# Optimization experiments

Measured on AMD Instinct MI355X. Metric: run time of the kernel, lower is better.

## Reference

```python
import jax, jax.numpy as jnp
import numpy as np

IN_FEATS = 64
OUT_FEATS = 64
HID = IN_FEATS * OUT_FEATS  # 4096, LSTM hidden size
N_NODES = 50000
N_EDGES = 800000
T = 3
NEG_SLOPE = 0.2


def setup_inputs() -> dict:
    key = jax.random.key(0)
    ks = jax.random.split(key, 12)
    node_embs = jax.random.normal(ks[0], (T, N_NODES, IN_FEATS), dtype=jnp.float32)
    mask = jax.random.normal(ks[1], (T, N_NODES), dtype=jnp.float32)
    edge_index = jax.random.randint(ks[2], (T, 2, N_EDGES), 0, N_NODES, dtype=jnp.int64)
    edge_weight = jax.random.uniform(ks[3], (T, N_EDGES), dtype=jnp.float32)
    # LSTMCell params (torch layout): gates order i,f,g,o
    s_ih = 1.0 / np.sqrt(HID)
    W_ih = jax.random.uniform(ks[4], (4 * HID, IN_FEATS), minval=-s_ih, maxval=s_ih, dtype=jnp.float32)
    W_hh = jax.random.uniform(ks[5], (4 * HID, HID), minval=-s_ih, maxval=s_ih, dtype=jnp.float32)
    b_ih = jax.random.uniform(ks[6], (4 * HID,), minval=-s_ih, maxval=s_ih, dtype=jnp.float32)
    b_hh = jax.random.uniform(ks[7], (4 * HID,), minval=-s_ih, maxval=s_ih, dtype=jnp.float32)
    # GCN init weights, uniform(-1/sqrt(out), 1/sqrt(out))
    s_w = 1.0 / np.sqrt(OUT_FEATS)
    W0 = jax.random.uniform(ks[8], (IN_FEATS, OUT_FEATS), minval=-s_w, maxval=s_w, dtype=jnp.float32)
    # GAT attention vector, split into src/dst halves
    att = jax.random.uniform(ks[9], (2, OUT_FEATS), minval=-s_w, maxval=s_w, dtype=jnp.float32)
    return {"node_embs": node_embs, "mask": mask, "edge_index": edge_index,
            "edge_weight": edge_weight, "W_ih": W_ih, "W_hh": W_hh,
            "b_ih": b_ih, "b_hh": b_hh, "W0": W0, "att": att}


def _lstm_cell(x, h, c, W_ih, W_hh, b_ih, b_hh):
    gates = W_ih @ x + b_ih + W_hh @ h + b_hh  # [4H]
    i, f, g, o = jnp.split(gates, 4)
    c2 = jax.nn.sigmoid(f) * c + jax.nn.sigmoid(i) * jnp.tanh(g)
    h2 = jax.nn.sigmoid(o) * jnp.tanh(c2)
    return h2, c2


def _gat_mp(x, src, dst, edge_w, W, att_l, att_r):
    h = x @ W  # [N, out]
    e = jax.nn.leaky_relu(h[src] @ att_l + h[dst] @ att_r, NEG_SLOPE)  # [E]
    m = jax.ops.segment_max(e, dst, num_segments=N_NODES)
    ex = jnp.exp(e - m[dst])
    denom = jax.ops.segment_sum(ex, dst, num_segments=N_NODES)
    alpha = ex / (denom[dst] + 1e-16)
    msg = (alpha * edge_w)[:, None] * h[src]  # [E, out]
    return jax.ops.segment_sum(msg, dst, num_segments=N_NODES)  # [N, out]


def reference(node_embs, mask, edge_index, edge_weight, W_ih, W_hh, b_ih, b_hh, W0, att):
    att_l, att_r = att[0], att[1]

    def step(carry, xs):
        h, c = carry
        x_t, mask_t, ei_t, ew_t = xs
        # input to weight-evolving LSTM: softmax-weighted node-feature mean -> [in_feats]
        w = jax.nn.softmax(mask_t)
        inp = jnp.einsum('n,nf->f', w, x_t)
        h2, c2 = _lstm_cell(inp, h, c, W_ih, W_hh, b_ih, b_hh)
        W = h2.reshape(IN_FEATS, OUT_FEATS)
        out = _gat_mp(x_t, ei_t[0], ei_t[1], ew_t, W, att_l, att_r)
        return (h2, c2), out

    init = (W0.reshape(-1), jnp.zeros((HID,), dtype=W0.dtype))
    _, out_seq = jax.lax.scan(step, init, (node_embs, mask, edge_index, edge_weight))
    return out_seq  # [T, N, out_feats]
```

## Files before the change

kernel.cpp:

```cpp
#include <hip/hip_runtime.h>
#include <hip/hip_fp16.h>
#include <math.h>

#define NN 50000
#define NE 800000
#define FEAT 64
#define HID 4096
#define NEG_SLOPE 0.2f
#define T_STEPS 3
#define SLOTS 64
#define NB 391
#define CAP 2560
#define CHUNK 4096
#define CHUNKS_PER_STEP ((NE + CHUNK - 1) / CHUNK)
#define FEAT_BLKS ((NN + 255) / 256)

__device__ __forceinline__ int pack_half2(float a, float b) {
    __half2 h = __floats2half2_rn(a, b);
    return *(int*)&h;
}
__device__ __forceinline__ float2 unpack_half2(int v) {
    __half2 h = *(__half2*)&v;
    return __half22float2(h);
}

__global__ void k_init(const float* __restrict__ W0, float* __restrict__ h0, float* __restrict__ c,
                       float* __restrict__ inp_acc, float* __restrict__ sumexp,
                       int* __restrict__ coarse_cnt) {
    int i = blockIdx.x * blockDim.x + threadIdx.x;
    if (i < HID) { h0[i] = W0[i]; c[i] = 0.f; }
    if (i < T_STEPS * FEAT) inp_acc[i] = 0.f;
    if (i < T_STEPS) sumexp[i] = 0.f;
    if (i < T_STEPS * NB) coarse_cnt[i] = 0;
}

__global__ void k_wsum_all(const float* __restrict__ node_embs, const float* __restrict__ mask,
                           float* __restrict__ sumexp, float* __restrict__ inp_acc) {
    int t = blockIdx.x >> 8;
    int blk = blockIdx.x & 255;
    const float* x_t = node_embs + (size_t)t * NN * FEAT;
    const float* mask_t = mask + (size_t)t * NN;
    int lane = threadIdx.x & 63;
    int wib = threadIdx.x >> 6;
    int gw = blk * 4 + wib;
    float acc = 0.f, se = 0.f;
    for (int n = gw; n < NN; n += 1024) {
        float w = expf(mask_t[n]);
        acc += w * x_t[(size_t)n * FEAT + lane];
        se += w;
    }
    __shared__ float sacc[4][FEAT];
    sacc[wib][lane] = acc;
    __syncthreads();
    if (wib == 0)
        atomicAdd(&inp_acc[t * FEAT + lane],
                  sacc[0][lane] + sacc[1][lane] + sacc[2][lane] + sacc[3][lane]);
    if (lane == 0) atomicAdd(&sumexp[t], se);
}

template <bool CVT>
__global__ __launch_bounds__(256) void k_lstm(
    const float* __restrict__ Wih, const float* __restrict__ Whh, __half* __restrict__ Whh_h,
    const float* __restrict__ bih, const float* __restrict__ bhh,
    const float* __restrict__ inp_acc_t, const float* __restrict__ sumexp_t,
    const float* __restrict__ h_old, float* __restrict__ h_new,
    float* __restrict__ c, float* __restrict__ Wbuf_t) {
    int lane = threadIdx.x & 63;
    int u = (blockIdx.x * blockDim.x + threadIdx.x) >> 6;
    if (u >= HID) return;
    float inp_l = inp_acc_t[lane] / (*sumexp_t);
    const float4* h4 = (const float4*)h_old;
    float g4[4];
    #pragma unroll
    for (int gi = 0; gi < 4; ++gi) {
        int row = u + gi * HID;
        float acc = 0.f;
        if (CVT) {
            const float4* wr = (const float4*)(Whh + (size_t)row * HID);
            int2* wh = (int2*)(Whh_h + (size_t)row * HID);
            #pragma unroll
            for (int cc = 0; cc < 16; ++cc) {
                float4 w = wr[cc * 64 + lane];
                float4 hv = h4[cc * 64 + lane];
                acc += w.x * hv.x + w.y * hv.y + w.z * hv.z + w.w * hv.w;
                int2 p;
                p.x = pack_half2(w.x, w.y);
                p.y = pack_half2(w.z, w.w);
                wh[cc * 64 + lane] = p;
            }
        } else {
            const int4* wr = (const int4*)(Whh_h + (size_t)row * HID);
            #pragma unroll
            for (int cc = 0; cc < 8; ++cc) {
                int4 w = wr[cc * 64 + lane];
                float2 wa = unpack_half2(w.x), wb = unpack_half2(w.y);
                float2 wc = unpack_half2(w.z), wd = unpack_half2(w.w);
                float4 hv0 = h4[(cc * 64 + lane) * 2];
                float4 hv1 = h4[(cc * 64 + lane) * 2 + 1];
                acc += wa.x * hv0.x + wa.y * hv0.y + wb.x * hv0.z + wb.y * hv0.w;
                acc += wc.x * hv1.x + wc.y * hv1.y + wd.x * hv1.z + wd.y * hv1.w;
            }
        }
        acc += Wih[(size_t)row * FEAT + lane] * inp_l;
        #pragma unroll
        for (int off = 32; off > 0; off >>= 1) acc += __shfl_xor(acc, off, 64);
        if (lane == 0) g4[gi] = acc + bih[row] + bhh[row];
    }
    if (lane == 0) {
        float si = 1.f / (1.f + expf(-g4[0]));
        float sf = 1.f / (1.f + expf(-g4[1]));
        float so = 1.f / (1.f + expf(-g4[3]));
        float c2 = sf * c[u] + si * tanhf(g4[2]);
        float h2 = so * tanhf(c2);
        c[u] = c2; h_new[u] = h2; Wbuf_t[u] = h2;
    }
}

__global__ __launch_bounds__(256) void k_feat_all(
    const float* __restrict__ node_embs, const float* __restrict__ Wbuf,
    const float* __restrict__ att, __half* __restrict__ hfeat,
    float* __restrict__ al, float* __restrict__ ar) {
    int t = blockIdx.x / FEAT_BLKS;
    int blk = blockIdx.x % FEAT_BLKS;
    __shared__ float Wl[HID];
    __shared__ float attS[2 * FEAT];
    for (int i = threadIdx.x; i < HID; i += 256) Wl[i] = Wbuf[t * HID + i];
    if (threadIdx.x < 2 * FEAT) attS[threadIdx.x] = att[threadIdx.x];
    __syncthreads();
    int n = blk * 256 + threadIdx.x;
    if (n >= NN) return;
    const float* x_t = node_embs + (size_t)t * NN * FEAT;
    float acc[FEAT];
    #pragma unroll
    for (int o = 0; o < FEAT; ++o) acc[o] = 0.f;
    const float4* x4 = (const float4*)(x_t + (size_t)n * FEAT);
    for (int k4 = 0; k4 < 16; ++k4) {
        float4 xv = x4[k4];
        const float* w0 = &Wl[(k4 * 4 + 0) * FEAT];
        const float* w1 = &Wl[(k4 * 4 + 1) * FEAT];
        const float* w2 = &Wl[(k4 * 4 + 2) * FEAT];
        const float* w3 = &Wl[(k4 * 4 + 3) * FEAT];
        #pragma unroll
        for (int o = 0; o < FEAT; ++o)
            acc[o] += xv.x * w0[o] + xv.y * w1[o] + xv.z * w2[o] + xv.w * w3[o];
    }
    float aL = 0.f, aR = 0.f;
    #pragma unroll
    for (int o = 0; o < FEAT; ++o) { aL += acc[o] * attS[o]; aR += acc[o] * attS[FEAT + o]; }
    size_t gn = (size_t)t * NN + n;
    int4* hf = (int4*)(hfeat + gn * FEAT);
    #pragma unroll
    for (int i = 0; i < 8; ++i) {
        int4 v;
        v.x = pack_half2(acc[8 * i + 0], acc[8 * i + 1]);
        v.y = pack_half2(acc[8 * i + 2], acc[8 * i + 3]);
        v.z = pack_half2(acc[8 * i + 4], acc[8 * i + 5]);
        v.w = pack_half2(acc[8 * i + 6], acc[8 * i + 7]);
        hf[i] = v;
    }
    al[gn] = aL; ar[gn] = aR;
}

__global__ __launch_bounds__(256) void k_part(
    const int* __restrict__ edge_index, const float* __restrict__ edge_weight,
    int* __restrict__ coarse_cnt, int2* __restrict__ coarse) {
    int t = blockIdx.x / CHUNKS_PER_STEP;
    int ch = blockIdx.x % CHUNKS_PER_STEP;
    int e0 = ch * CHUNK;
    int eN = (e0 + CHUNK <= NE) ? CHUNK : (NE - e0);
    const int* src = edge_index + (size_t)t * 2 * NE;
    const int* dst = src + NE;
    const float* ew = edge_weight + (size_t)t * NE;
    int tid = threadIdx.x;

    __shared__ int hist[NB], offs[NB], baseg[NB], cursor[NB];
    __shared__ int sc[256];
    __shared__ int2 stag[CHUNK];

    for (int i = tid; i < NB; i += 256) hist[i] = 0;
    __syncthreads();
    for (int k = tid; k < eN; k += 256) {
        int d = dst[e0 + k];
        atomicAdd(&hist[d >> 7], 1);
    }
    __syncthreads();
    int a0 = (2 * tid < NB) ? hist[2 * tid] : 0;
    int a1 = (2 * tid + 1 < NB) ? hist[2 * tid + 1] : 0;
    sc[tid] = a0 + a1;
    __syncthreads();
    for (int off = 1; off < 256; off <<= 1) {
        int v = (tid >= off) ? sc[tid - off] : 0;
        __syncthreads();
        sc[tid] += v;
        __syncthreads();
    }
    int excl = (tid == 0) ? 0 : sc[tid - 1];
    if (2 * tid < NB)     { offs[2 * tid] = excl;      cursor[2 * tid] = excl; }
    if (2 * tid + 1 < NB) { offs[2 * tid + 1] = excl + a0; cursor[2 * tid + 1] = excl + a0; }
    __syncthreads();
    for (int k = tid; k < eN; k += 256) {
        int d = dst[e0 + k], s = src[e0 + k];
        float wv = ew[e0 + k];
        int cb = d >> 7, doff = d & 127;
        int p = atomicAdd(&cursor[cb], 1);
        stag[p] = make_int2(s | (doff << 16) | (cb << 23), __float_as_int(wv));
    }
    __syncthreads();
    for (int cb = tid; cb < NB; cb += 256) {
        int cnum = hist[cb];
        baseg[cb] = cnum ? atomicAdd(&coarse_cnt[t * NB + cb], cnum) : 0;
    }
    __syncthreads();
    for (int j = tid; j < eN; j += 256) {
        int2 r = stag[j];
        int cb = ((unsigned)r.x) >> 23;
        int gpos = baseg[cb] + (j - offs[cb]);
        if (gpos < CAP)
            coarse[((size_t)(t * NB + cb)) * CAP + gpos] = r;
    }
}

__global__ __launch_bounds__(512) void k_gat(
    const int* __restrict__ coarse_cnt, const int2* __restrict__ coarse,
    const float* __restrict__ al, const float* __restrict__ ar,
    const __half* __restrict__ hfeat, float* __restrict__ out) {
    int t = blockIdx.x / NB;
    int cb = blockIdx.x % NB;
    int n0 = cb << 7;
    int tid = threadIdx.x;
    __shared__ int fine[128 * SLOTS];
    __shared__ int fcnt[128];
    for (int i = tid; i < 128; i += 512) fcnt[i] = 0;
    __syncthreads();
    int m = coarse_cnt[t * NB + cb];
    if (m > CAP) m = CAP;
    const int2* reg = coarse + ((size_t)(t * NB + cb)) * CAP;
    for (int k = tid; k < m; k += 512) {
        int2 r = reg[k];
        int doff = (r.x >> 16) & 127;
        int p = atomicAdd(&fcnt[doff], 1);
        if (p < SLOTS) {
            unsigned int eh = (unsigned int)__half_as_ushort(__float2half_rn(__int_as_float(r.y)));
            fine[doff * SLOTS + p] = (r.x & 0xffff) | (int)(eh << 16);
        }
    }
    __syncthreads();
    int lane = tid & 63, w = tid >> 6;
    const float* al_t = al + (size_t)t * NN;
    const __half* hf_t = hfeat + (size_t)t * NN * FEAT;
    int sub = lane >> 4;
    int fl = (lane & 15) * 4;
    for (int doff = w; doff < 128; doff += 8) {
        int row = n0 + doff;
        if (row >= NN) break;
        int cn = fcnt[doff]; if (cn > SLOTS) cn = SLOTS;
        float ard = ar[(size_t)t * NN + row];
        float4 acc = make_float4(0.f, 0.f, 0.f, 0.f);
        float psum = 0.f;
        for (int i = sub; i < cn; i += 4) {
            int r = fine[doff * SLOTS + i];
            int s = r & 0xffff;
            float ewv = __half2float(__ushort_as_half((unsigned short)((unsigned int)r >> 16)));
            float e = al_t[s] + ard;
            e = e >= 0.f ? e : NEG_SLOPE * e;
            float p = expf(e);
            psum += p;
            float pe = p * ewv;
            int2 hv2 = *(const int2*)(hf_t + (size_t)s * FEAT + fl);
            float2 ha = unpack_half2(hv2.x), hb = unpack_half2(hv2.y);
            acc.x += pe * ha.x; acc.y += pe * ha.y;
            acc.z += pe * hb.x; acc.w += pe * hb.y;
        }
        acc.x += __shfl_xor(acc.x, 16, 64); acc.y += __shfl_xor(acc.y, 16, 64);
        acc.z += __shfl_xor(acc.z, 16, 64); acc.w += __shfl_xor(acc.w, 16, 64);
        psum  += __shfl_xor(psum, 16, 64);
        acc.x += __shfl_xor(acc.x, 32, 64); acc.y += __shfl_xor(acc.y, 32, 64);
        acc.z += __shfl_xor(acc.z, 32, 64); acc.w += __shfl_xor(acc.w, 32, 64);
        psum  += __shfl_xor(psum, 32, 64);
        float inv = 1.f / (psum + 1e-16f);
        if (sub == 0)
            *(float4*)(out + ((size_t)t * NN + row) * FEAT + fl) =
                make_float4(acc.x * inv, acc.y * inv, acc.z * inv, acc.w * inv);
    }
}

extern "C" void kernel_launch(void* const* d_in, const int* in_sizes, int n_in,
                              void* d_out, int out_size, void* d_ws, size_t ws_size,
                              hipStream_t stream) {
    const float* node_embs   = (const float*)d_in[0];
    const float* mask        = (const float*)d_in[1];
    const int*   edge_index  = (const int*)d_in[2];
    const float* edge_weight = (const float*)d_in[3];
    const float* Wih         = (const float*)d_in[4];
    const float* Whh         = (const float*)d_in[5];
    const float* bih         = (const float*)d_in[6];
    const float* bhh         = (const float*)d_in[7];
    const float* W0          = (const float*)d_in[8];
    const float* att         = (const float*)d_in[9];
    float* out = (float*)d_out;
    float* ws  = (float*)d_ws;

    float*  h0       = ws;
    float*  h1       = ws + 4096;
    float*  c_state  = ws + 8192;
    float*  sumexp   = ws + 12288;
    float*  inp_acc  = ws + 12292;
    float*  Wbuf     = ws + 12544;
    float*  al       = ws + 24832;
    float*  ar       = ws + 174832;
    int*    ccnt     = (int*)(ws + 324832);
    int2*   coarse   = (int2*)(ws + 326016);
    __half* Whh_h    = (__half*)(ws + 6331776);
    __half* hfeat    = (__half*)(ws + 39886208);

    k_init<<<16, 256, 0, stream>>>(W0, h0, c_state, inp_acc, sumexp, ccnt);
    k_wsum_all<<<T_STEPS * 256, 256, 0, stream>>>(node_embs, mask, sumexp, inp_acc);

    float* hc = h0;
    for (int t = 0; t < T_STEPS; ++t) {
        float* hn = (hc == h0) ? h1 : h0;
        if (t == 0)
            k_lstm<true><<<HID / 4, 256, 0, stream>>>(Wih, Whh, Whh_h, bih, bhh,
                                                      inp_acc + t * FEAT, sumexp + t,
                                                      hc, hn, c_state, Wbuf + (size_t)t * HID);
        else
            k_lstm<false><<<HID / 4, 256, 0, stream>>>(Wih, Whh, Whh_h, bih, bhh,
                                                       inp_acc + t * FEAT, sumexp + t,
                                                       hc, hn, c_state, Wbuf + (size_t)t * HID);
        hc = hn;
    }

    k_feat_all<<<T_STEPS * FEAT_BLKS, 256, 0, stream>>>(node_embs, Wbuf, att, hfeat, al, ar);
    k_part<<<T_STEPS * CHUNKS_PER_STEP, 256, 0, stream>>>(edge_index, edge_weight, ccnt, coarse);
    k_gat<<<T_STEPS * NB, 512, 0, stream>>>(ccnt, coarse, al, ar, hfeat, out);
}
```

Baseline: 354.2 us.

## Merge prep kernels and overlap per-step feature transform with next LSTM step

Edge partitioning, the weighted node mean and a standalone fp32-to-fp16 conversion of W_hh now run as disjoint block ranges of a single prep kernel, so these independent phases share one launch and fill the GPU together. The feature transform for step t is fused into the same launch as the LSTM for step t+1, letting the memory-bound LSTM matvec overlap with the node feature GEMM. Initialization moves to a device memcpy and memset, and the first LSTM step no longer converts W_hh itself. This adds a separate full pass over W_hh for the conversion and makes block scheduling of the mixed launches harder to predict.

```diff
diff --git a/kernel.cpp b/kernel.cpp
--- a/kernel.cpp
+++ b/kernel.cpp
@@ -14,6 +14,9 @@
 #define CHUNK 4096
 #define CHUNKS_PER_STEP ((NE + CHUNK - 1) / CHUNK)
 #define FEAT_BLKS ((NN + 255) / 256)
+#define PART_BLKS (T_STEPS * CHUNKS_PER_STEP)
+#define WSUM_BLKS (T_STEPS * 256)
+#define CVT_BLKS 4096
 
 __device__ __forceinline__ int pack_half2(float a, float b) {
     __half2 h = __floats2half2_rn(a, b);
@@ -24,71 +27,163 @@
     return __half22float2(h);
 }
 
-__global__ void k_init(const float* __restrict__ W0, float* __restrict__ h0, float* __restrict__ c,
-                       float* __restrict__ inp_acc, float* __restrict__ sumexp,
-                       int* __restrict__ coarse_cnt) {
-    int i = blockIdx.x * blockDim.x + threadIdx.x;
-    if (i < HID) { h0[i] = W0[i]; c[i] = 0.f; }
-    if (i < T_STEPS * FEAT) inp_acc[i] = 0.f;
-    if (i < T_STEPS) sumexp[i] = 0.f;
-    if (i < T_STEPS * NB) coarse_cnt[i] = 0;
-}
-
-__global__ void k_wsum_all(const float* __restrict__ node_embs, const float* __restrict__ mask,
-                           float* __restrict__ sumexp, float* __restrict__ inp_acc) {
-    int t = blockIdx.x >> 8;
-    int blk = blockIdx.x & 255;
-    const float* x_t = node_embs + (size_t)t * NN * FEAT;
-    const float* mask_t = mask + (size_t)t * NN;
-    int lane = threadIdx.x & 63;
-    int wib = threadIdx.x >> 6;
-    int gw = blk * 4 + wib;
-    float acc = 0.f, se = 0.f;
-    for (int n = gw; n < NN; n += 1024) {
-        float w = expf(mask_t[n]);
-        acc += w * x_t[(size_t)n * FEAT + lane];
-        se += w;
+__global__ __launch_bounds__(256) void k_prep(
+    const int* __restrict__ edge_index, const float* __restrict__ edge_weight,
+    const float* __restrict__ node_embs, const float* __restrict__ mask,
+    const float* __restrict__ Whh, __half* __restrict__ Whh_h,
+    float* __restrict__ sumexp, float* __restrict__ inp_acc,
+    int* __restrict__ coarse_cnt, int2* __restrict__ coarse) {
+    __shared__ char smem[40448];
+    int bid = blockIdx.x;
+    int tid = threadIdx.x;
+    if (bid < PART_BLKS) {
+        int t = bid / CHUNKS_PER_STEP;
+        int ch = bid % CHUNKS_PER_STEP;
+        int e0 = ch * CHUNK;
+        int eN = (e0 + CHUNK <= NE) ? CHUNK : (NE - e0);
+        const int* src = edge_index + (size_t)t * 2 * NE;
+        const int* dst = src + NE;
+        const float* ew = edge_weight + (size_t)t * NE;
+        int2* stag  = (int2*)smem;
+        int* hist   = (int*)(smem + 32768);
+        int* offs   = (int*)(smem + 34332);
+        int* baseg  = (int*)(smem + 35896);
+        int* cursor = (int*)(smem + 37460);
+        int* sc     = (int*)(smem + 39024);
+        for (int i = tid; i < NB; i += 256) hist[i] = 0;
+        __syncthreads();
+        for (int k = tid; k < eN; k += 256) atomicAdd(&hist[dst[e0 + k] >> 7], 1);
+        __syncthreads();
+        int a0 = (2 * tid < NB) ? hist[2 * tid] : 0;
+        int a1 = (2 * tid + 1 < NB) ? hist[2 * tid + 1] : 0;
+        sc[tid] = a0 + a1;
+        __syncthreads();
+        for (int off = 1; off < 256; off <<= 1) {
+            int v = (tid >= off) ? sc[tid - off] : 0;
+            __syncthreads();
+            sc[tid] += v;
+            __syncthreads();
+        }
+        int excl = (tid == 0) ? 0 : sc[tid - 1];
+        if (2 * tid < NB)     { offs[2 * tid] = excl;          cursor[2 * tid] = excl; }
+        if (2 * tid + 1 < NB) { offs[2 * tid + 1] = excl + a0; cursor[2 * tid + 1] = excl + a0; }
+        __syncthreads();
+        for (int k = tid; k < eN; k += 256) {
+            int d = dst[e0 + k], s = src[e0 + k];
+            float wv = ew[e0 + k];
+            int cb = d >> 7, doff = d & 127;
+            int p = atomicAdd(&cursor[cb], 1);
+            stag[p] = make_int2(s | (doff << 16) | (cb << 23), __float_as_int(wv));
+        }
+        __syncthreads();
+        for (int cb = tid; cb < NB; cb += 256) {
+            int cnum = hist[cb];
+            baseg[cb] = cnum ? atomicAdd(&coarse_cnt[t * NB + cb], cnum) : 0;
+        }
+        __syncthreads();
+        for (int j = tid; j < eN; j += 256) {
+            int2 r = stag[j];
+            int cb = ((unsigned)r.x) >> 23;
+            int gpos = baseg[cb] + (j - offs[cb]);
+            if (gpos < CAP)
+                coarse[((size_t)(t * NB + cb)) * CAP + gpos] = r;
+        }
+    } else if (bid < PART_BLKS + WSUM_BLKS) {
+        int wid = bid - PART_BLKS;
+        int t = wid >> 8;
+        int blk = wid & 255;
+        const float* x_t = node_embs + (size_t)t * NN * FEAT;
+        const float* mask_t = mask + (size_t)t * NN;
+        int lane = tid & 63;
+        int wib = tid >> 6;
+        int gw = blk * 4 + wib;
+        float acc = 0.f, se = 0.f;
+        for (int n = gw; n < NN; n += 1024) {
+            float w = expf(mask_t[n]);
+            acc += w * x_t[(size_t)n * FEAT + lane];
+            se += w;
+        }
+        float (*sacc)[FEAT] = (float (*)[FEAT])smem;
+        sacc[wib][lane] = acc;
+        __syncthreads();
+        if (wib == 0)
+            atomicAdd(&inp_acc[t * FEAT + lane],
+                      sacc[0][lane] + sacc[1][lane] + sacc[2][lane] + sacc[3][lane]);
+        if (lane == 0) atomicAdd(&sumexp[t], se);
+    } else {
+        int cid = bid - (PART_BLKS + WSUM_BLKS);
+        const float4* s4 = (const float4*)Whh;
+        int2* d2 = (int2*)Whh_h;
+        int base = cid * 4096 + tid;
+        #pragma unroll
+        for (int j = 0; j < 16; ++j) {
+            int idx = base + j * 256;
+            float4 v = s4[idx];
+            int2 p;
+            p.x = pack_half2(v.x, v.y);
+            p.y = pack_half2(v.z, v.w);
+            d2[idx] = p;
+        }
     }
-    __shared__ float sacc[4][FEAT];
-    sacc[wib][lane] = acc;
-    __syncthreads();
-    if (wib == 0)
-        atomicAdd(&inp_acc[t * FEAT + lane],
-                  sacc[0][lane] + sacc[1][lane] + sacc[2][lane] + sacc[3][lane]);
-    if (lane == 0) atomicAdd(&sumexp[t], se);
-}
-
-template <bool CVT>
-__global__ __launch_bounds__(256) void k_lstm(
-    const float* __restrict__ Wih, const float* __restrict__ Whh, __half* __restrict__ Whh_h,
+}
+
+__global__ __launch_bounds__(256) void k_lstm_feat(
+    const float* __restrict__ Wih, const __half* __restrict__ Whh_h,
     const float* __restrict__ bih, const float* __restrict__ bhh,
     const float* __restrict__ inp_acc_t, const float* __restrict__ sumexp_t,
     const float* __restrict__ h_old, float* __restrict__ h_new,
-    float* __restrict__ c, float* __restrict__ Wbuf_t) {
-    int lane = threadIdx.x & 63;
-    int u = (blockIdx.x * blockDim.x + threadIdx.x) >> 6;
-    if (u >= HID) return;
-    float inp_l = inp_acc_t[lane] / (*sumexp_t);
-    const float4* h4 = (const float4*)h_old;
-    float g4[4];
-    #pragma unroll
-    for (int gi = 0; gi < 4; ++gi) {
-        int row = u + gi * HID;
-        float acc = 0.f;
-        if (CVT) {
-            const float4* wr = (const float4*)(Whh + (size_t)row * HID);
-            int2* wh = (int2*)(Whh_h + (size_t)row * HID);
+    float* __restrict__ c, float* __restrict__ Wbuf_lt,
+    const float* __restrict__ node_embs, const float* __restrict__ Wbuf_ft,
+    const float* __restrict__ att, __half* __restrict__ hfeat_ft,
+    float* __restrict__ al_ft, float* __restrict__ ar_ft, int nfeat) {
+    __shared__ float Wl[HID];
+    __shared__ float attS[2 * FEAT];
+    int bid = blockIdx.x;
+    if (bid < nfeat) {
+        for (int i = threadIdx.x; i < HID; i += 256) Wl[i] = Wbuf_ft[i];
+        if (threadIdx.x < 2 * FEAT) attS[threadIdx.x] = att[threadIdx.x];
+        __syncthreads();
+        int n = bid * 256 + threadIdx.x;
+        if (n >= NN) return;
+        float acc[FEAT];
+        #pragma unroll
+        for (int o = 0; o < FEAT; ++o) acc[o] = 0.f;
+        const float4* x4 = (const float4*)(node_embs + (size_t)n * FEAT);
+        for (int k4 = 0; k4 < 16; ++k4) {
+            float4 xv = x4[k4];
+            const float* w0 = &Wl[(k4 * 4 + 0) * FEAT];
+            const float* w1 = &Wl[(k4 * 4 + 1) * FEAT];
+            const float* w2 = &Wl[(k4 * 4 + 2) * FEAT];
+            const float* w3 = &Wl[(k4 * 4 + 3) * FEAT];
             #pragma unroll
-            for (int cc = 0; cc < 16; ++cc) {
-                float4 w = wr[cc * 64 + lane];
-                float4 hv = h4[cc * 64 + lane];
-                acc += w.x * hv.x + w.y * hv.y + w.z * hv.z + w.w * hv.w;
-                int2 p;
-                p.x = pack_half2(w.x, w.y);
-                p.y = pack_half2(w.z, w.w);
-                wh[cc * 64 + lane] = p;
-            }
-        } else {
+            for (int o = 0; o < FEAT; ++o)
+                acc[o] += xv.x * w0[o] + xv.y * w1[o] + xv.z * w2[o] + xv.w * w3[o];
+        }
+        float aL = 0.f, aR = 0.f;
+        #pragma unroll
+        for (int o = 0; o < FEAT; ++o) { aL += acc[o] * attS[o]; aR += acc[o] * attS[FEAT + o]; }
+        int4* hf = (int4*)(hfeat_ft + (size_t)n * FEAT);
+        #pragma unroll
+        for (int i = 0; i < 8; ++i) {
+            int4 v;
+            v.x = pack_half2(acc[8 * i + 0], acc[8 * i + 1]);
+            v.y = pack_half2(acc[8 * i + 2], acc[8 * i + 3]);
+            v.z = pack_half2(acc[8 * i + 4], acc[8 * i + 5]);
+            v.w = pack_half2(acc[8 * i + 6], acc[8 * i + 7]);
+            hf[i] = v;
+        }
+        al_ft[n] = aL; ar_ft[n] = aR;
+    } else {
+        int lane = threadIdx.x & 63;
+        int u = (((bid - nfeat) * 256 + (int)threadIdx.x)) >> 6;
+        if (u >= HID) return;
+        float inp_l = inp_acc_t[lane] / (*sumexp_t);
+        const float4* h4 = (const float4*)h_old;
+        float g4[4];
+        #pragma unroll
+        for (int gi = 0; gi < 4; ++gi) {
+            int row = u + gi * HID;
+            float acc = 0.f;
             const int4* wr = (const int4*)(Whh_h + (size_t)row * HID);
             #pragma unroll
             for (int cc = 0; cc < 8; ++cc) {
@@ -100,123 +195,19 @@
                 acc += wa.x * hv0.x + wa.y * hv0.y + wb.x * hv0.z + wb.y * hv0.w;
                 acc += wc.x * hv1.x + wc.y * hv1.y + wd.x * hv1.z + wd.y * hv1.w;
             }
-        }
-        acc += Wih[(size_t)row * FEAT + lane] * inp_l;
-        #pragma unroll
-        for (int off = 32; off > 0; off >>= 1) acc += __shfl_xor(acc, off, 64);
-        if (lane == 0) g4[gi] = acc + bih[row] + bhh[row];
-    }
-    if (lane == 0) {
-        float si = 1.f / (1.f + expf(-g4[0]));
-        float sf = 1.f / (1.f + expf(-g4[1]));
-        float so = 1.f / (1.f + expf(-g4[3]));
-        float c2 = sf * c[u] + si * tanhf(g4[2]);
-        float h2 = so * tanhf(c2);
-        c[u] = c2; h_new[u] = h2; Wbuf_t[u] = h2;
-    }
-}
-
-__global__ __launch_bounds__(256) void k_feat_all(
-    const float* __restrict__ node_embs, const float* __restrict__ Wbuf,
-    const float* __restrict__ att, __half* __restrict__ hfeat,
-    float* __restrict__ al, float* __restrict__ ar) {
-    int t = blockIdx.x / FEAT_BLKS;
-    int blk = blockIdx.x % FEAT_BLKS;
-    __shared__ float Wl[HID];
-    __shared__ float attS[2 * FEAT];
-    for (int i = threadIdx.x; i < HID; i += 256) Wl[i] = Wbuf[t * HID + i];
-    if (threadIdx.x < 2 * FEAT) attS[threadIdx.x] = att[threadIdx.x];
-    __syncthreads();
-    int n = blk * 256 + threadIdx.x;
-    if (n >= NN) return;
-    const float* x_t = node_embs + (size_t)t * NN * FEAT;
-    float acc[FEAT];
-    #pragma unroll
-    for (int o = 0; o < FEAT; ++o) acc[o] = 0.f;
-    const float4* x4 = (const float4*)(x_t + (size_t)n * FEAT);
-    for (int k4 = 0; k4 < 16; ++k4) {
-        float4 xv = x4[k4];
-        const float* w0 = &Wl[(k4 * 4 + 0) * FEAT];
-        const float* w1 = &Wl[(k4 * 4 + 1) * FEAT];
-        const float* w2 = &Wl[(k4 * 4 + 2) * FEAT];
-        const float* w3 = &Wl[(k4 * 4 + 3) * FEAT];
-        #pragma unroll
-        for (int o = 0; o < FEAT; ++o)
-            acc[o] += xv.x * w0[o] + xv.y * w1[o] + xv.z * w2[o] + xv.w * w3[o];
-    }
-    float aL = 0.f, aR = 0.f;
-    #pragma unroll
-    for (int o = 0; o < FEAT; ++o) { aL += acc[o] * attS[o]; aR += acc[o] * attS[FEAT + o]; }
-    size_t gn = (size_t)t * NN + n;
-    int4* hf = (int4*)(hfeat + gn * FEAT);
-    #pragma unroll
-    for (int i = 0; i < 8; ++i) {
-        int4 v;
-        v.x = pack_half2(acc[8 * i + 0], acc[8 * i + 1]);
-        v.y = pack_half2(acc[8 * i + 2], acc[8 * i + 3]);
-        v.z = pack_half2(acc[8 * i + 4], acc[8 * i + 5]);
-        v.w = pack_half2(acc[8 * i + 6], acc[8 * i + 7]);
-        hf[i] = v;
-    }
-    al[gn] = aL; ar[gn] = aR;
-}
-
-__global__ __launch_bounds__(256) void k_part(
-    const int* __restrict__ edge_index, const float* __restrict__ edge_weight,
-    int* __restrict__ coarse_cnt, int2* __restrict__ coarse) {
-    int t = blockIdx.x / CHUNKS_PER_STEP;
-    int ch = blockIdx.x % CHUNKS_PER_STEP;
-    int e0 = ch * CHUNK;
-    int eN = (e0 + CHUNK <= NE) ? CHUNK : (NE - e0);
-    const int* src = edge_index + (size_t)t * 2 * NE;
-    const int* dst = src + NE;
-    const float* ew = edge_weight + (size_t)t * NE;
-    int tid = threadIdx.x;
-
-    __shared__ int hist[NB], offs[NB], baseg[NB], cursor[NB];
-    __shared__ int sc[256];
-    __shared__ int2 stag[CHUNK];
-
-    for (int i = tid; i < NB; i += 256) hist[i] = 0;
-    __syncthreads();
-    for (int k = tid; k < eN; k += 256) {
-        int d = dst[e0 + k];
-        atomicAdd(&hist[d >> 7], 1);
-    }
-    __syncthreads();
-    int a0 = (2 * tid < NB) ? hist[2 * tid] : 0;
-    int a1 = (2 * tid + 1 < NB) ? hist[2 * tid + 1] : 0;
-    sc[tid] = a0 + a1;
-    __syncthreads();
-    for (int off = 1; off < 256; off <<= 1) {
-        int v = (tid >= off) ? sc[tid - off] : 0;
-        __syncthreads();
-        sc[tid] += v;
-        __syncthreads();
-    }
-    int excl = (tid == 0) ? 0 : sc[tid - 1];
-    if (2 * tid < NB)     { offs[2 * tid] = excl;      cursor[2 * tid] = excl; }
-    if (2 * tid + 1 < NB) { offs[2 * tid + 1] = excl + a0; cursor[2 * tid + 1] = excl + a0; }
-    __syncthreads();
-    for (int k = tid; k < eN; k += 256) {
-        int d = dst[e0 + k], s = src[e0 + k];
-        float wv = ew[e0 + k];
-        int cb = d >> 7, doff = d & 127;
-        int p = atomicAdd(&cursor[cb], 1);
-        stag[p] = make_int2(s | (doff << 16) | (cb << 23), __float_as_int(wv));
-    }
-    __syncthreads();
-    for (int cb = tid; cb < NB; cb += 256) {
-        int cnum = hist[cb];
-        baseg[cb] = cnum ? atomicAdd(&coarse_cnt[t * NB + cb], cnum) : 0;
-    }
-    __syncthreads();
-    for (int j = tid; j < eN; j += 256) {
-        int2 r = stag[j];
-        int cb = ((unsigned)r.x) >> 23;
-        int gpos = baseg[cb] + (j - offs[cb]);
-        if (gpos < CAP)
-            coarse[((size_t)(t * NB + cb)) * CAP + gpos] = r;
+            acc += Wih[(size_t)row * FEAT + lane] * inp_l;
+            #pragma unroll
+            for (int off = 32; off > 0; off >>= 1) acc += __shfl_xor(acc, off, 64);
+            if (lane == 0) g4[gi] = acc + bih[row] + bhh[row];
+        }
+        if (lane == 0) {
+            float si = 1.f / (1.f + expf(-g4[0]));
+            float sf = 1.f / (1.f + expf(-g4[1]));
+            float so = 1.f / (1.f + expf(-g4[3]));
+            float c2 = sf * c[u] + si * tanhf(g4[2]);
+            float h2 = so * tanhf(c2);
+            c[u] = c2; h_new[u] = h2; Wbuf_lt[u] = h2;
+        }
     }
 }
 
@@ -305,32 +296,35 @@
     float*  c_state  = ws + 8192;
     float*  sumexp   = ws + 12288;
     float*  inp_acc  = ws + 12292;
-    float*  Wbuf     = ws + 12544;
-    float*  al       = ws + 24832;
-    float*  ar       = ws + 174832;
-    int*    ccnt     = (int*)(ws + 324832);
-    int2*   coarse   = (int2*)(ws + 326016);
-    __half* Whh_h    = (__half*)(ws + 6331776);
-    __half* hfeat    = (__half*)(ws + 39886208);
-
-    k_init<<<16, 256, 0, stream>>>(W0, h0, c_state, inp_acc, sumexp, ccnt);
-    k_wsum_all<<<T_STEPS * 256, 256, 0, stream>>>(node_embs, mask, sumexp, inp_acc);
-
-    float* hc = h0;
-    for (int t = 0; t < T_STEPS; ++t) {
-        float* hn = (hc == h0) ? h1 : h0;
-        if (t == 0)
-            k_lstm<true><<<HID / 4, 256, 0, stream>>>(Wih, Whh, Whh_h, bih, bhh,
-                                                      inp_acc + t * FEAT, sumexp + t,
-                                                      hc, hn, c_state, Wbuf + (size_t)t * HID);
-        else
-            k_lstm<false><<<HID / 4, 256, 0, stream>>>(Wih, Whh, Whh_h, bih, bhh,
-                                                       inp_acc + t * FEAT, sumexp + t,
-                                                       hc, hn, c_state, Wbuf + (size_t)t * HID);
-        hc = hn;
-    }
-
-    k_feat_all<<<T_STEPS * FEAT_BLKS, 256, 0, stream>>>(node_embs, Wbuf, att, hfeat, al, ar);
-    k_part<<<T_STEPS * CHUNKS_PER_STEP, 256, 0, stream>>>(edge_index, edge_weight, ccnt, coarse);
+    int*    ccnt     = (int*)(ws + 12484);
+    float*  Wbuf     = ws + 13660;
+    float*  al       = ws + 25948;
+    float*  ar       = ws + 175948;
+    int2*   coarse   = (int2*)(ws + 325948);
+    __half* Whh_h    = (__half*)(ws + 6331708);
+    __half* hfeat    = (__half*)(ws + 39886140);
+
+    hipMemcpyAsync(h0, W0, HID * sizeof(float), hipMemcpyDeviceToDevice, stream);
+    hipMemsetAsync(ws + 8192, 0, (size_t)(13657 - 8192) * sizeof(float), stream);
+
+    k_prep<<<PART_BLKS + WSUM_BLKS + CVT_BLKS, 256, 0, stream>>>(
+        edge_index, edge_weight, node_embs, mask, Whh, Whh_h, sumexp, inp_acc, ccnt, coarse);
+
+    k_lstm_feat<<<1024, 256, 0, stream>>>(
+        Wih, Whh_h, bih, bhh, inp_acc + 0 * FEAT, sumexp + 0, h0, h1, c_state, Wbuf + 0 * HID,
+        node_embs, Wbuf, att, hfeat, al, ar, 0);
+    k_lstm_feat<<<FEAT_BLKS + 1024, 256, 0, stream>>>(
+        Wih, Whh_h, bih, bhh, inp_acc + 1 * FEAT, sumexp + 1, h1, h0, c_state, Wbuf + 1 * HID,
+        node_embs + (size_t)0 * NN * FEAT, Wbuf + 0 * HID, att,
+        hfeat + (size_t)0 * NN * FEAT, al + (size_t)0 * NN, ar + (size_t)0 * NN, FEAT_BLKS);
+    k_lstm_feat<<<FEAT_BLKS + 1024, 256, 0, stream>>>(
+        Wih, Whh_h, bih, bhh, inp_acc + 2 * FEAT, sumexp + 2, h0, h1, c_state, Wbuf + 2 * HID,
+        node_embs + (size_t)1 * NN * FEAT, Wbuf + 1 * HID, att,
+        hfeat + (size_t)1 * NN * FEAT, al + (size_t)1 * NN, ar + (size_t)1 * NN, FEAT_BLKS);
+    k_lstm_feat<<<FEAT_BLKS, 256, 0, stream>>>(
+        Wih, Whh_h, bih, bhh, inp_acc + 2 * FEAT, sumexp + 2, h1, h0, c_state, Wbuf + 2 * HID,
+        node_embs + (size_t)2 * NN * FEAT, Wbuf + 2 * HID, att,
+        hfeat + (size_t)2 * NN * FEAT, al + (size_t)2 * NN, ar + (size_t)2 * NN, FEAT_BLKS);
+
     k_gat<<<T_STEPS * NB, 512, 0, stream>>>(ccnt, coarse, al, ar, hfeat, out);
 }
```

New measurement: 359.3 us. No clear change (+1.4%).
